# Optimization experiments

Hardware: AMD Instinct MI355X
Metric: run time of the kernel (lower is better)

The kernel has to match this reference:

```python
import jax, jax.numpy as jnp
import numpy as np

B, S = 32, 2048
DIM_ACTION = 32
DIM_STRUCT = 64
HIDDEN = 128  # mlp_hidden_dim default = dim_action * 4
EPS = 1e-12   # F.normalize eps


def l2norm(t):
    n = jnp.linalg.norm(t, axis=-1, keepdims=True)
    return t / jnp.maximum(n, EPS)


def setup_inputs() -> dict:
    key = jax.random.key(0)
    ks = jax.random.split(key, 9)
    sd = lambda fan_in: 1.0 / np.sqrt(fan_in)
    inp = {
        "actions": jax.random.normal(ks[0], (B, S, DIM_ACTION), dtype=jnp.float32),
        # MLP: dim_action -> hidden -> hidden -> dim_structure^2 (depth=2 hidden relu layers)
        "w0": jax.random.uniform(ks[1], (DIM_ACTION, HIDDEN), jnp.float32, -sd(DIM_ACTION), sd(DIM_ACTION)),
        "b0": jnp.zeros((HIDDEN,), jnp.float32),
        "w1": jax.random.uniform(ks[2], (HIDDEN, HIDDEN), jnp.float32, -sd(HIDDEN), sd(HIDDEN)),
        "b1": jnp.zeros((HIDDEN,), jnp.float32),
        "w2": jax.random.uniform(ks[3], (HIDDEN, DIM_STRUCT * DIM_STRUCT), jnp.float32, -sd(HIDDEN), sd(HIDDEN)),
        "b2": jnp.zeros((DIM_STRUCT * DIM_STRUCT,), jnp.float32),
        # RNN init hidden parameter [1, dim_structure], ~N(0, 0.01)
        "init_hidden": jax.random.normal(ks[4], (1, DIM_STRUCT), dtype=jnp.float32) * 0.01,
    }
    return inp


def reference(actions, w0, b0, w1, b1, w2, b2, init_hidden):
    # MLP to transitions: [B, S, d*d]
    h = jax.nn.relu(jnp.einsum("bsa,ah->bsh", actions, w0) + b0)
    h = jax.nn.relu(jnp.einsum("bsh,hk->bsk", h, w1) + b1)
    t = jnp.einsum("bsh,ho->bso", h, w2) + b2
    transitions = t.reshape(B, S, DIM_STRUCT, DIM_STRUCT)  # [B, S, i, j]

    # RNN: hidden_{t+1} = l2norm(relu(hidden_t @ T_t)), scanned over seq
    hidden0 = jnp.broadcast_to(l2norm(init_hidden), (B, DIM_STRUCT))

    def step(hidden, trans):  # trans: [B, i, j]
        hidden = jnp.einsum("bi,bij->bj", hidden, trans)
        hidden = l2norm(jax.nn.relu(hidden))
        return hidden, hidden

    trans_seq = jnp.swapaxes(transitions, 0, 1)  # [S, B, i, j]
    _, hiddens = jax.lax.scan(step, hidden0, trans_seq)  # [S, B, d]
    return jnp.swapaxes(hiddens, 0, 1)  # [B, S, d]
```

## Files before the change

### kernel.cpp

```cpp
#include <hip/hip_runtime.h>

#define B_ 32
#define S_ 2048
#define DA 32
#define DH 128
#define DS 64
#define DS2 4096
#define TKK 16

template <int CTRL>
__device__ __forceinline__ float dpp_add(float x) {
  int t = __builtin_amdgcn_update_dpp(0, __float_as_int(x), CTRL, 0xF, 0xF, true);
  return x + __int_as_float(t);
}
__device__ __forceinline__ float row_sum16(float x) {
  x = dpp_add<0xB1>(x);
  x = dpp_add<0x4E>(x);
  x = dpp_add<0x141>(x);
  x = dpp_add<0x140>(x);
  return x;
}

__device__ __forceinline__ void gl2lds16(const float* g, float* l) {
  __builtin_amdgcn_global_load_lds(
      (const __attribute__((address_space(1))) void*)g,
      (__attribute__((address_space(3))) void*)l, 16, 0, 0);
}

struct SharedRnn {
  float4 ring[6][16][64];
  int flags[6];
  int cons;
};
struct SharedGemm {
  float As[2][TKK][128];
  float Bs[2][TKK][128];
};
struct SharedMlp {
  float a_t[DA][64];
  float w0_l[DA][DH];
  float h0t[DH][64];
};
union SharedU {
  SharedRnn r;
  SharedGemm g;
  SharedMlp m;
};

__device__ __forceinline__ void mlp_tile(
    const float* __restrict__ actions, const float* __restrict__ w0,
    const float* __restrict__ b0, const float* __restrict__ w1,
    const float* __restrict__ b1, float* __restrict__ h1t,
    int s_base, int M, int m0, SharedMlp& sm, int tid)
{
#pragma unroll
  for (int q = 0; q < 2; ++q) {
    int g = tid + 256 * q;
    int tok = g >> 3, kq = g & 7;
    int tl = m0 + tok;
    int b = tl & 31, s = s_base + (tl >> 5);
    float4 v = *(const float4*)(actions + ((size_t)b * S_ + s) * DA + 4 * kq);
    sm.a_t[4 * kq + 0][tok] = v.x; sm.a_t[4 * kq + 1][tok] = v.y;
    sm.a_t[4 * kq + 2][tok] = v.z; sm.a_t[4 * kq + 3][tok] = v.w;
  }
#pragma unroll
  for (int q = 0; q < 4; ++q) {
    int g = tid + 256 * q;
    ((float4*)&sm.w0_l[0][0])[g] = ((const float4*)w0)[g];
  }
  __syncthreads();

  const int tm = tid & 15;
  const int tn = tid >> 4;

  float acc[4][8];
#pragma unroll
  for (int mi = 0; mi < 4; ++mi)
#pragma unroll
    for (int ni = 0; ni < 8; ++ni) acc[mi][ni] = 0.f;

#pragma unroll 4
  for (int k = 0; k < DA; ++k) {
    float4 a4 = *(const float4*)&sm.a_t[k][4 * tm];
    float4 wa = *(const float4*)&sm.w0_l[k][8 * tn];
    float4 wb = *(const float4*)&sm.w0_l[k][8 * tn + 4];
    float av[4] = {a4.x, a4.y, a4.z, a4.w};
    float wv[8] = {wa.x, wa.y, wa.z, wa.w, wb.x, wb.y, wb.z, wb.w};
#pragma unroll
    for (int mi = 0; mi < 4; ++mi)
#pragma unroll
      for (int ni = 0; ni < 8; ++ni) acc[mi][ni] += av[mi] * wv[ni];
  }
  {
    float4 ba = *(const float4*)(b0 + 8 * tn);
    float4 bb = *(const float4*)(b0 + 8 * tn + 4);
    float bv[8] = {ba.x, ba.y, ba.z, ba.w, bb.x, bb.y, bb.z, bb.w};
#pragma unroll
    for (int mi = 0; mi < 4; ++mi)
#pragma unroll
      for (int ni = 0; ni < 8; ++ni)
        sm.h0t[8 * tn + ni][4 * tm + mi] = fmaxf(acc[mi][ni] + bv[ni], 0.f);
  }
  __syncthreads();

  float acc1[4][8];
#pragma unroll
  for (int mi = 0; mi < 4; ++mi)
#pragma unroll
    for (int ni = 0; ni < 8; ++ni) acc1[mi][ni] = 0.f;

#pragma unroll 4
  for (int k = 0; k < DH; ++k) {
    float4 h4 = *(const float4*)&sm.h0t[k][4 * tm];
    float4 wa = *(const float4*)(w1 + (size_t)k * DH + 8 * tn);
    float4 wb = *(const float4*)(w1 + (size_t)k * DH + 8 * tn + 4);
    float av[4] = {h4.x, h4.y, h4.z, h4.w};
    float wv[8] = {wa.x, wa.y, wa.z, wa.w, wb.x, wb.y, wb.z, wb.w};
#pragma unroll
    for (int mi = 0; mi < 4; ++mi)
#pragma unroll
      for (int ni = 0; ni < 8; ++ni) acc1[mi][ni] += av[mi] * wv[ni];
  }
  {
    float4 ba = *(const float4*)(b1 + 8 * tn);
    float4 bb = *(const float4*)(b1 + 8 * tn + 4);
    float bv[8] = {ba.x, ba.y, ba.z, ba.w, bb.x, bb.y, bb.z, bb.w};
#pragma unroll
    for (int ni = 0; ni < 8; ++ni) {
      float4 o;
      o.x = fmaxf(acc1[0][ni] + bv[ni], 0.f);
      o.y = fmaxf(acc1[1][ni] + bv[ni], 0.f);
      o.z = fmaxf(acc1[2][ni] + bv[ni], 0.f);
      o.w = fmaxf(acc1[3][ni] + bv[ni], 0.f);
      *(float4*)(h1t + (size_t)(8 * tn + ni) * M + m0 + 4 * tm) = o;
    }
  }
}

__device__ __forceinline__ void trans_tile(
    const float* __restrict__ h1t, const float* __restrict__ w2,
    const float* __restrict__ b2, float* __restrict__ trans,
    int M, int n0, int m0, SharedGemm& sg, int tid)
{
  const int w  = tid >> 6;
  const int lw = tid & 63;

  auto aload = [&](int t, int buf) {
#pragma unroll
    for (int ii = 0; ii < 2; ++ii) {
      const int i = 2 * w + ii;
      const int kr = 2 * i + (lw >> 5);
      const int c4 = 4 * (lw & 31);
      gl2lds16(h1t + (size_t)(t * TKK + kr) * M + m0 + c4, &sg.As[buf][2 * i][0]);
      gl2lds16(w2 + (size_t)(t * TKK + kr) * DS2 + n0 + c4, &sg.Bs[buf][2 * i][0]);
    }
  };

  aload(0, 0);

  const int mg = tid >> 4;
  const int ng = tid & 15;
  float acc[8][8];
#pragma unroll
  for (int mi = 0; mi < 8; ++mi)
#pragma unroll
    for (int ni = 0; ni < 8; ++ni) acc[mi][ni] = 0.f;

  int buf = 0;
  for (int t = 0; t < DH / TKK; ++t) {
    __syncthreads();
    if (t < DH / TKK - 1) aload(t + 1, buf ^ 1);
#pragma unroll
    for (int k = 0; k < TKK; ++k) {
      float4 a0 = *(const float4*)&sg.As[buf][k][8 * mg];
      float4 a1 = *(const float4*)&sg.As[buf][k][8 * mg + 4];
      float av[8] = {a0.x, a0.y, a0.z, a0.w, a1.x, a1.y, a1.z, a1.w};
      float4 b0v = *(const float4*)&sg.Bs[buf][k][4 * ng];
      float4 b1v = *(const float4*)&sg.Bs[buf][k][64 + 4 * ng];
      float bv[8] = {b0v.x, b0v.y, b0v.z, b0v.w, b1v.x, b1v.y, b1v.z, b1v.w};
#pragma unroll
      for (int mi = 0; mi < 8; ++mi)
#pragma unroll
        for (int ni = 0; ni < 8; ++ni) acc[mi][ni] += av[mi] * bv[ni];
    }
    buf ^= 1;
  }

  float4 bb0 = *(const float4*)(b2 + n0 + 4 * ng);
  float4 bb1 = *(const float4*)(b2 + n0 + 64 + 4 * ng);
  float bv[8] = {bb0.x, bb0.y, bb0.z, bb0.w, bb1.x, bb1.y, bb1.z, bb1.w};
#pragma unroll
  for (int mi = 0; mi < 8; ++mi) {
    float* dst = trans + (size_t)(m0 + 8 * mg + mi) * DS2 + n0;
#pragma unroll
    for (int q = 0; q < 2; ++q) {
      float4 o;
      o.x = acc[mi][4 * q + 0] + bv[4 * q + 0];
      o.y = acc[mi][4 * q + 1] + bv[4 * q + 1];
      o.z = acc[mi][4 * q + 2] + bv[4 * q + 2];
      o.w = acc[mi][4 * q + 3] + bv[4 * q + 3];
      *(float4*)(dst + 64 * q + 4 * ng) = o;
    }
  }
}

__global__ __launch_bounds__(256) void k_mlp01(
    const float* __restrict__ actions, const float* __restrict__ w0,
    const float* __restrict__ b0, const float* __restrict__ w1,
    const float* __restrict__ b1, float* __restrict__ h1t,
    int s_base, int M)
{
  __shared__ SharedMlp sm;
  mlp_tile(actions, w0, b0, w1, b1, h1t, s_base, M, blockIdx.x * 64, sm,
           threadIdx.x);
}

__global__ __launch_bounds__(256, 1) void k_comb(
    const float* __restrict__ actions, const float* __restrict__ w0,
    const float* __restrict__ b0, const float* __restrict__ w1,
    const float* __restrict__ b1, const float* __restrict__ w2,
    const float* __restrict__ b2, const float* __restrict__ init_hidden,
    float* __restrict__ trans0, float* __restrict__ trans1,
    float* __restrict__ h1t0, float* __restrict__ h1t1,
    float* __restrict__ hstate, float* __restrict__ out,
    int c, int SC, int nch)
{
  __shared__ SharedU sh;
  const int tid = threadIdx.x;
  const int M = SC * 32;

  if (blockIdx.x >= 32) {
    const int bi = blockIdx.x - 32;
    if (c < nch) {
      const float* h1t = (c & 1) ? h1t1 : h1t0;
      float* trans = (c & 1) ? trans1 : trans0;
      const int NJ = (M / 128) * (DS2 / 128);
      for (int j = bi; j < NJ; j += 224) {
        const int mt = j >> 5, nt = j & 31;
        trans_tile(h1t, w2, b2, trans, M, nt * 128, mt * 128, sh.g, tid);
        __syncthreads();
      }
      if (c + 1 < nch) {
        __syncthreads();
        float* h1n = ((c + 1) & 1) ? h1t1 : h1t0;
        for (int j = bi; j < M / 64; j += 224) {
          mlp_tile(actions, w0, b0, w1, b1, h1n, (c + 1) * SC, M, j * 64,
                   sh.m, tid);
          __syncthreads();
        }
      }
    }
    return;
  }

  if (c == 0) return;
  const int cc = c - 1;
  const float* trans = (cc & 1) ? trans1 : trans0;
  const int s_base = cc * SC;
  const int wv = tid >> 6;
  const int lane = tid & 63;
  const int b = blockIdx.x;

  if (tid < 6) sh.r.flags[tid] = 0;
  if (tid == 6) sh.r.cons = 0;
  __syncthreads();

  const float* base = trans + (size_t)b * DS2;

  if (wv > 0) {
    const int p = wv - 1;
    int prev = -1;
    for (int s = p; s < SC; s += 3) {
      while (s - __hip_atomic_load(&sh.r.cons, __ATOMIC_RELAXED,
                                   __HIP_MEMORY_SCOPE_WORKGROUP) > 5)
        __builtin_amdgcn_s_sleep(2);
      const int slot = s % 6;
      const float* g = base + (size_t)s * (32 * DS2) + 4 * lane;
      float* l = (float*)&sh.r.ring[slot][0][0];
#pragma unroll
      for (int q = 0; q < 16; ++q)
        gl2lds16(g + q * 256, l + q * 256);
      if (prev >= 0) {
        asm volatile("s_waitcnt vmcnt(16)" ::: "memory");
        __hip_atomic_store(&sh.r.flags[prev % 6], prev + 1, __ATOMIC_RELAXED,
                           __HIP_MEMORY_SCOPE_WORKGROUP);
      }
      prev = s;
    }
    if (prev >= 0) {
      asm volatile("s_waitcnt vmcnt(0)" ::: "memory");
      __hip_atomic_store(&sh.r.flags[prev % 6], prev + 1, __ATOMIC_RELAXED,
                         __HIP_MEMORY_SCOPE_WORKGROUP);
    }
  } else {
    const int d = lane >> 4;
    const int cq = lane & 15;
    const bool d1 = (d & 1), d2 = (d & 2);
    const int pb = lane & 48;

    float4 hq;
    if (cc == 0) {
      hq = *(const float4*)(init_hidden + 4 * cq);
      float ss0 = row_sum16(hq.x * hq.x + hq.y * hq.y + hq.z * hq.z + hq.w * hq.w);
      float iv0 = 1.0f / fmaxf(sqrtf(ss0), 1e-12f);
      hq.x *= iv0; hq.y *= iv0; hq.z *= iv0; hq.w *= iv0;
    } else {
      hq = *(const float4*)(hstate + b * DS + 4 * cq);
    }
    float inv_prev = 1.0f;

    float* outp = out + ((size_t)b * S_ + s_base) * DS + 4 * cq;
    int fpre = -1;
    for (int s = 0; s < SC; ++s) {
      const int slot = s % 6;
      if (fpre < s + 1) {
        while (__hip_atomic_load(&sh.r.flags[slot], __ATOMIC_ACQUIRE,
                                 __HIP_MEMORY_SCOPE_WORKGROUP) < s + 1)
          __builtin_amdgcn_s_sleep(0);
      }
      fpre = __hip_atomic_load(&sh.r.flags[(s + 1) % 6], __ATOMIC_ACQUIRE,
                               __HIP_MEMORY_SCOPE_WORKGROUP);

      float hsel = d2 ? (d1 ? hq.w : hq.z) : (d1 ? hq.y : hq.x);
      float ax = 0.f, ay = 0.f, az = 0.f, aw = 0.f;
#pragma unroll
      for (int q = 0; q < 16; ++q) {
        float4 t4 = sh.r.ring[slot][q][lane];
        float hb = __shfl(hsel, pb + q, 64);
        ax += hb * t4.x; ay += hb * t4.y;
        az += hb * t4.z; aw += hb * t4.w;
      }
      __hip_atomic_store(&sh.r.cons, s + 1, __ATOMIC_RELAXED,
                         __HIP_MEMORY_SCOPE_WORKGROUP);

      ax += __shfl_xor(ax, 16, 64); ax += __shfl_xor(ax, 32, 64);
      ay += __shfl_xor(ay, 16, 64); ay += __shfl_xor(ay, 32, 64);
      az += __shfl_xor(az, 16, 64); az += __shfl_xor(az, 32, 64);
      aw += __shfl_xor(aw, 16, 64); aw += __shfl_xor(aw, 32, 64);
      hq.x = fmaxf(ax * inv_prev, 0.f);
      hq.y = fmaxf(ay * inv_prev, 0.f);
      hq.z = fmaxf(az * inv_prev, 0.f);
      hq.w = fmaxf(aw * inv_prev, 0.f);
      float ss = row_sum16(hq.x * hq.x + hq.y * hq.y + hq.z * hq.z + hq.w * hq.w);
      float inv = 1.0f / fmaxf(sqrtf(ss), 1e-12f);
      if (d == 0) {
        float4 o;
        o.x = hq.x * inv; o.y = hq.y * inv; o.z = hq.z * inv; o.w = hq.w * inv;
        *(float4*)(outp + (size_t)s * DS) = o;
      }
      inv_prev = inv;
    }
    if (d == 0) {
      float4 o;
      o.x = hq.x * inv_prev; o.y = hq.y * inv_prev;
      o.z = hq.z * inv_prev; o.w = hq.w * inv_prev;
      *(float4*)(hstate + b * DS + 4 * cq) = o;
    }
  }
}

extern "C" void kernel_launch(void* const* d_in, const int* in_sizes, int n_in,
                              void* d_out, int out_size, void* d_ws, size_t ws_size,
                              hipStream_t stream) {
  const float* actions     = (const float*)d_in[0];
  const float* w0          = (const float*)d_in[1];
  const float* b0          = (const float*)d_in[2];
  const float* w1          = (const float*)d_in[3];
  const float* b1          = (const float*)d_in[4];
  const float* w2          = (const float*)d_in[5];
  const float* b2          = (const float*)d_in[6];
  const float* init_hidden = (const float*)d_in[7];
  float* out = (float*)d_out;

  int SC = 2048;
  while (SC > 4) {
    size_t need = 2 * ((size_t)SC * 32 * DS2 * 4 + (size_t)SC * 32 * DH * 4)
                + (size_t)B_ * DS * 4;
    if (need <= ws_size) break;
    SC >>= 1;
  }
  float* trans0 = (float*)d_ws;
  float* trans1 = trans0 + (size_t)SC * 32 * DS2;
  float* h1t0   = trans1 + (size_t)SC * 32 * DS2;
  float* h1t1   = h1t0 + (size_t)SC * 32 * DH;
  float* hstate = h1t1 + (size_t)SC * 32 * DH;

  const int M = SC * 32;
  const int nch = S_ / SC;

  hipLaunchKernelGGL(k_mlp01, dim3(M / 64), dim3(256), 0, stream,
                     actions, w0, b0, w1, b1, h1t0, 0, M);
  for (int c = 0; c <= nch; ++c) {
    hipLaunchKernelGGL(k_comb, dim3(256), dim3(256), 0, stream,
                       actions, w0, b0, w1, b1, w2, b2, init_hidden,
                       trans0, trans1, h1t0, h1t1, hstate, out, c, SC, nch);
  }
}
```

Baseline: 1.620 ms.

## Double block size to 512 threads with split-K GEMM and LDS reduction

Launches the combined and MLP kernels with 512 threads. In the transition GEMM the K dimension of each tile is split between two 256-thread halves, and their partial sums are combined through a new shared-memory buffer. The MLP tile spreads the same work across more threads, and the GEMM tile index is permuted across blocks. The RNN blocks keep only three loader waves, so the extra waves sit idle. The change adds LDS usage and an extra reduction and barrier per tile in exchange for more waves per CU to hide latency.

```diff
diff --git a/kernel.cpp b/kernel.cpp
--- a/kernel.cpp
+++ b/kernel.cpp
@@ -35,6 +35,7 @@
 struct SharedGemm {
   float As[2][TKK][128];
   float Bs[2][TKK][128];
+  float4 part[256][17];
 };
 struct SharedMlp {
   float a_t[DA][64];
@@ -53,10 +54,8 @@
     const float* __restrict__ b1, float* __restrict__ h1t,
     int s_base, int M, int m0, SharedMlp& sm, int tid)
 {
-#pragma unroll
-  for (int q = 0; q < 2; ++q) {
-    int g = tid + 256 * q;
-    int tok = g >> 3, kq = g & 7;
+  {
+    int tok = tid >> 3, kq = tid & 7;
     int tl = m0 + tok;
     int b = tl & 31, s = s_base + (tl >> 5);
     float4 v = *(const float4*)(actions + ((size_t)b * S_ + s) * DA + 4 * kq);
@@ -64,8 +63,8 @@
     sm.a_t[4 * kq + 2][tok] = v.z; sm.a_t[4 * kq + 3][tok] = v.w;
   }
 #pragma unroll
-  for (int q = 0; q < 4; ++q) {
-    int g = tid + 256 * q;
+  for (int q = 0; q < 2; ++q) {
+    int g = tid + 512 * q;
     ((float4*)&sm.w0_l[0][0])[g] = ((const float4*)w0)[g];
   }
   __syncthreads();
@@ -73,66 +72,62 @@
   const int tm = tid & 15;
   const int tn = tid >> 4;
 
-  float acc[4][8];
+  float acc[4][4];
 #pragma unroll
   for (int mi = 0; mi < 4; ++mi)
 #pragma unroll
-    for (int ni = 0; ni < 8; ++ni) acc[mi][ni] = 0.f;
+    for (int ni = 0; ni < 4; ++ni) acc[mi][ni] = 0.f;
 
 #pragma unroll 4
   for (int k = 0; k < DA; ++k) {
     float4 a4 = *(const float4*)&sm.a_t[k][4 * tm];
-    float4 wa = *(const float4*)&sm.w0_l[k][8 * tn];
-    float4 wb = *(const float4*)&sm.w0_l[k][8 * tn + 4];
+    float4 w4 = *(const float4*)&sm.w0_l[k][4 * tn];
     float av[4] = {a4.x, a4.y, a4.z, a4.w};
-    float wv[8] = {wa.x, wa.y, wa.z, wa.w, wb.x, wb.y, wb.z, wb.w};
+    float wv[4] = {w4.x, w4.y, w4.z, w4.w};
 #pragma unroll
     for (int mi = 0; mi < 4; ++mi)
 #pragma unroll
-      for (int ni = 0; ni < 8; ++ni) acc[mi][ni] += av[mi] * wv[ni];
+      for (int ni = 0; ni < 4; ++ni) acc[mi][ni] += av[mi] * wv[ni];
   }
   {
-    float4 ba = *(const float4*)(b0 + 8 * tn);
-    float4 bb = *(const float4*)(b0 + 8 * tn + 4);
-    float bv[8] = {ba.x, ba.y, ba.z, ba.w, bb.x, bb.y, bb.z, bb.w};
+    float4 b4 = *(const float4*)(b0 + 4 * tn);
+    float bv[4] = {b4.x, b4.y, b4.z, b4.w};
 #pragma unroll
     for (int mi = 0; mi < 4; ++mi)
 #pragma unroll
-      for (int ni = 0; ni < 8; ++ni)
-        sm.h0t[8 * tn + ni][4 * tm + mi] = fmaxf(acc[mi][ni] + bv[ni], 0.f);
+      for (int ni = 0; ni < 4; ++ni)
+        sm.h0t[4 * tn + ni][4 * tm + mi] = fmaxf(acc[mi][ni] + bv[ni], 0.f);
   }
   __syncthreads();
 
-  float acc1[4][8];
+  float acc1[4][4];
 #pragma unroll
   for (int mi = 0; mi < 4; ++mi)
 #pragma unroll
-    for (int ni = 0; ni < 8; ++ni) acc1[mi][ni] = 0.f;
+    for (int ni = 0; ni < 4; ++ni) acc1[mi][ni] = 0.f;
 
 #pragma unroll 4
   for (int k = 0; k < DH; ++k) {
     float4 h4 = *(const float4*)&sm.h0t[k][4 * tm];
-    float4 wa = *(const float4*)(w1 + (size_t)k * DH + 8 * tn);
-    float4 wb = *(const float4*)(w1 + (size_t)k * DH + 8 * tn + 4);
+    float4 w4 = *(const float4*)(w1 + (size_t)k * DH + 4 * tn);
     float av[4] = {h4.x, h4.y, h4.z, h4.w};
-    float wv[8] = {wa.x, wa.y, wa.z, wa.w, wb.x, wb.y, wb.z, wb.w};
+    float wv[4] = {w4.x, w4.y, w4.z, w4.w};
 #pragma unroll
     for (int mi = 0; mi < 4; ++mi)
 #pragma unroll
-      for (int ni = 0; ni < 8; ++ni) acc1[mi][ni] += av[mi] * wv[ni];
+      for (int ni = 0; ni < 4; ++ni) acc1[mi][ni] += av[mi] * wv[ni];
   }
   {
-    float4 ba = *(const float4*)(b1 + 8 * tn);
-    float4 bb = *(const float4*)(b1 + 8 * tn + 4);
-    float bv[8] = {ba.x, ba.y, ba.z, ba.w, bb.x, bb.y, bb.z, bb.w};
-#pragma unroll
-    for (int ni = 0; ni < 8; ++ni) {
+    float4 b4 = *(const float4*)(b1 + 4 * tn);
+    float bv[4] = {b4.x, b4.y, b4.z, b4.w};
+#pragma unroll
+    for (int ni = 0; ni < 4; ++ni) {
       float4 o;
       o.x = fmaxf(acc1[0][ni] + bv[ni], 0.f);
       o.y = fmaxf(acc1[1][ni] + bv[ni], 0.f);
       o.z = fmaxf(acc1[2][ni] + bv[ni], 0.f);
       o.w = fmaxf(acc1[3][ni] + bv[ni], 0.f);
-      *(float4*)(h1t + (size_t)(8 * tn + ni) * M + m0 + 4 * tm) = o;
+      *(float4*)(h1t + (size_t)(4 * tn + ni) * M + m0 + 4 * tm) = o;
     }
   }
 }
@@ -146,20 +141,18 @@
   const int lw = tid & 63;
 
   auto aload = [&](int t, int buf) {
-#pragma unroll
-    for (int ii = 0; ii < 2; ++ii) {
-      const int i = 2 * w + ii;
-      const int kr = 2 * i + (lw >> 5);
-      const int c4 = 4 * (lw & 31);
-      gl2lds16(h1t + (size_t)(t * TKK + kr) * M + m0 + c4, &sg.As[buf][2 * i][0]);
-      gl2lds16(w2 + (size_t)(t * TKK + kr) * DS2 + n0 + c4, &sg.Bs[buf][2 * i][0]);
-    }
+    const int kr = 2 * w + (lw >> 5);
+    const int c4 = 4 * (lw & 31);
+    gl2lds16(h1t + (size_t)(t * TKK + kr) * M + m0 + c4, &sg.As[buf][2 * w][0]);
+    gl2lds16(w2 + (size_t)(t * TKK + kr) * DS2 + n0 + c4, &sg.Bs[buf][2 * w][0]);
   };
 
   aload(0, 0);
 
-  const int mg = tid >> 4;
-  const int ng = tid & 15;
+  const int sub = tid & 255;
+  const int khalf = tid >> 8;
+  const int mg = sub >> 4;
+  const int ng = sub & 15;
   float acc[8][8];
 #pragma unroll
   for (int mi = 0; mi < 8; ++mi)
@@ -167,11 +160,13 @@
     for (int ni = 0; ni < 8; ++ni) acc[mi][ni] = 0.f;
 
   int buf = 0;
+  const int kb = 8 * khalf;
   for (int t = 0; t < DH / TKK; ++t) {
     __syncthreads();
     if (t < DH / TKK - 1) aload(t + 1, buf ^ 1);
 #pragma unroll
-    for (int k = 0; k < TKK; ++k) {
+    for (int k8 = 0; k8 < 8; ++k8) {
+      const int k = kb + k8;
       float4 a0 = *(const float4*)&sg.As[buf][k][8 * mg];
       float4 a1 = *(const float4*)&sg.As[buf][k][8 * mg + 4];
       float av[8] = {a0.x, a0.y, a0.z, a0.w, a1.x, a1.y, a1.z, a1.w};
@@ -186,25 +181,41 @@
     buf ^= 1;
   }
 
-  float4 bb0 = *(const float4*)(b2 + n0 + 4 * ng);
-  float4 bb1 = *(const float4*)(b2 + n0 + 64 + 4 * ng);
-  float bv[8] = {bb0.x, bb0.y, bb0.z, bb0.w, bb1.x, bb1.y, bb1.z, bb1.w};
-#pragma unroll
-  for (int mi = 0; mi < 8; ++mi) {
-    float* dst = trans + (size_t)(m0 + 8 * mg + mi) * DS2 + n0;
-#pragma unroll
-    for (int q = 0; q < 2; ++q) {
-      float4 o;
-      o.x = acc[mi][4 * q + 0] + bv[4 * q + 0];
-      o.y = acc[mi][4 * q + 1] + bv[4 * q + 1];
-      o.z = acc[mi][4 * q + 2] + bv[4 * q + 2];
-      o.w = acc[mi][4 * q + 3] + bv[4 * q + 3];
-      *(float4*)(dst + 64 * q + 4 * ng) = o;
-    }
-  }
-}
-
-__global__ __launch_bounds__(256) void k_mlp01(
+  __syncthreads();
+  if (khalf) {
+#pragma unroll
+    for (int mi = 0; mi < 8; ++mi) {
+      sg.part[sub][2 * mi] =
+          make_float4(acc[mi][0], acc[mi][1], acc[mi][2], acc[mi][3]);
+      sg.part[sub][2 * mi + 1] =
+          make_float4(acc[mi][4], acc[mi][5], acc[mi][6], acc[mi][7]);
+    }
+  }
+  __syncthreads();
+  if (!khalf) {
+    float4 bb0 = *(const float4*)(b2 + n0 + 4 * ng);
+    float4 bb1 = *(const float4*)(b2 + n0 + 64 + 4 * ng);
+    float bv[8] = {bb0.x, bb0.y, bb0.z, bb0.w, bb1.x, bb1.y, bb1.z, bb1.w};
+#pragma unroll
+    for (int mi = 0; mi < 8; ++mi) {
+      float4 p0 = sg.part[sub][2 * mi];
+      float4 p1 = sg.part[sub][2 * mi + 1];
+      float pv[8] = {p0.x, p0.y, p0.z, p0.w, p1.x, p1.y, p1.z, p1.w};
+      float* dst = trans + (size_t)(m0 + 8 * mg + mi) * DS2 + n0;
+#pragma unroll
+      for (int q = 0; q < 2; ++q) {
+        float4 o;
+        o.x = acc[mi][4 * q + 0] + pv[4 * q + 0] + bv[4 * q + 0];
+        o.y = acc[mi][4 * q + 1] + pv[4 * q + 1] + bv[4 * q + 1];
+        o.z = acc[mi][4 * q + 2] + pv[4 * q + 2] + bv[4 * q + 2];
+        o.w = acc[mi][4 * q + 3] + pv[4 * q + 3] + bv[4 * q + 3];
+        *(float4*)(dst + 64 * q + 4 * ng) = o;
+      }
+    }
+  }
+}
+
+__global__ __launch_bounds__(512) void k_mlp01(
     const float* __restrict__ actions, const float* __restrict__ w0,
     const float* __restrict__ b0, const float* __restrict__ w1,
     const float* __restrict__ b1, float* __restrict__ h1t,
@@ -215,7 +226,7 @@
            threadIdx.x);
 }
 
-__global__ __launch_bounds__(256, 1) void k_comb(
+__global__ __launch_bounds__(512, 1) void k_comb(
     const float* __restrict__ actions, const float* __restrict__ w0,
     const float* __restrict__ b0, const float* __restrict__ w1,
     const float* __restrict__ b1, const float* __restrict__ w2,
@@ -230,7 +241,8 @@
   const int M = SC * 32;
 
   if (blockIdx.x >= 32) {
-    const int bi = blockIdx.x - 32;
+    const int x = blockIdx.x - 32;
+    const int bi = (x & 7) * 28 + (x >> 3);
     if (c < nch) {
       const float* h1t = (c & 1) ? h1t1 : h1t0;
       float* trans = (c & 1) ? trans1 : trans0;
@@ -268,29 +280,31 @@
   const float* base = trans + (size_t)b * DS2;
 
   if (wv > 0) {
-    const int p = wv - 1;
-    int prev = -1;
-    for (int s = p; s < SC; s += 3) {
-      while (s - __hip_atomic_load(&sh.r.cons, __ATOMIC_RELAXED,
-                                   __HIP_MEMORY_SCOPE_WORKGROUP) > 5)
-        __builtin_amdgcn_s_sleep(2);
-      const int slot = s % 6;
-      const float* g = base + (size_t)s * (32 * DS2) + 4 * lane;
-      float* l = (float*)&sh.r.ring[slot][0][0];
-#pragma unroll
-      for (int q = 0; q < 16; ++q)
-        gl2lds16(g + q * 256, l + q * 256);
+    if (wv <= 3) {
+      const int p = wv - 1;
+      int prev = -1;
+      for (int s = p; s < SC; s += 3) {
+        while (s - __hip_atomic_load(&sh.r.cons, __ATOMIC_RELAXED,
+                                     __HIP_MEMORY_SCOPE_WORKGROUP) > 5)
+          __builtin_amdgcn_s_sleep(2);
+        const int slot = s % 6;
+        const float* g = base + (size_t)s * (32 * DS2) + 4 * lane;
+        float* l = (float*)&sh.r.ring[slot][0][0];
+#pragma unroll
+        for (int q = 0; q < 16; ++q)
+          gl2lds16(g + q * 256, l + q * 256);
+        if (prev >= 0) {
+          asm volatile("s_waitcnt vmcnt(16)" ::: "memory");
+          __hip_atomic_store(&sh.r.flags[prev % 6], prev + 1, __ATOMIC_RELAXED,
+                             __HIP_MEMORY_SCOPE_WORKGROUP);
+        }
+        prev = s;
+      }
       if (prev >= 0) {
-        asm volatile("s_waitcnt vmcnt(16)" ::: "memory");
+        asm volatile("s_waitcnt vmcnt(0)" ::: "memory");
         __hip_atomic_store(&sh.r.flags[prev % 6], prev + 1, __ATOMIC_RELAXED,
                            __HIP_MEMORY_SCOPE_WORKGROUP);
       }
-      prev = s;
-    }
-    if (prev >= 0) {
-      asm volatile("s_waitcnt vmcnt(0)" ::: "memory");
-      __hip_atomic_store(&sh.r.flags[prev % 6], prev + 1, __ATOMIC_RELAXED,
-                         __HIP_MEMORY_SCOPE_WORKGROUP);
     }
   } else {
     const int d = lane >> 4;
@@ -388,10 +402,10 @@
   const int M = SC * 32;
   const int nch = S_ / SC;
 
-  hipLaunchKernelGGL(k_mlp01, dim3(M / 64), dim3(256), 0, stream,
+  hipLaunchKernelGGL(k_mlp01, dim3(M / 64), dim3(512), 0, stream,
                      actions, w0, b0, w1, b1, h1t0, 0, M);
   for (int c = 0; c <= nch; ++c) {
-    hipLaunchKernelGGL(k_comb, dim3(256), dim3(256), 0, stream,
+    hipLaunchKernelGGL(k_comb, dim3(256), dim3(512), 0, stream,
                        actions, w0, b0, w1, b1, w2, b2, init_hidden,
                        trans0, trans1, h1t0, h1t1, hstate, out, c, SC, nch);
   }
```

Result: no change. 1.593 ms (-1.7%).
